# Performance work log

Hardware: AMD Instinct MI355X
Metric: run time of the kernel (lower is better)

## Reference

```python
import jax, jax.numpy as jnp
import numpy as np

NORM_EPS = 1e-6


def setup_inputs() -> dict:
    key = jax.random.key(0)
    k1, k2 = jax.random.split(key)
    in_features, out_features = 4096, 4096
    x = jax.random.normal(k1, (2, 2048, in_features), dtype=jnp.float32)
    scale = 1.0 / np.sqrt(in_features)
    weight = jax.random.normal(k2, (out_features, in_features), dtype=jnp.float32) * scale
    norm_weight = jnp.ones((in_features,), dtype=jnp.float32)
    return {"x": x, "weight": weight, "norm_weight": norm_weight}


def reference(x, weight, norm_weight):
    # RMSNorm over the last dim
    rms = jnp.sqrt(jnp.mean(x * x, axis=-1, keepdims=True) + NORM_EPS)
    x_n = x / rms * norm_weight
    # ternary weight quantization (absmean scale alpha)
    alpha = jnp.maximum(jnp.mean(jnp.abs(weight)), 1e-10)
    w_q = jnp.clip(jnp.round(weight / alpha), -1.0, 1.0)
    # per-token int8 activation quantization (absmax scale gamma)
    gamma = jnp.maximum(jnp.max(jnp.abs(x_n), axis=-1, keepdims=True), 1e-10)
    x_q = jnp.clip(jnp.round(x_n * 127.0 / gamma), -128.0, 127.0)
    # rescaled matmul: y = x_q @ w_q.T * (alpha * gamma / 127)
    y = jnp.einsum('bsk,nk->bsn', x_q, w_q) * (alpha * gamma / 127.0)
    return y
```

## Files before the change

kernel.cpp:

```cpp
#include <hip/hip_runtime.h>
#include <cstdint>
#include <cstddef>


#define KD 4096
#define MD 4096
#define ND 4096

#define WBLK 512

typedef int i32x4 __attribute__((ext_vector_type(4)));

__device__ __forceinline__ void gl2lds16(const signed char* g, signed char* l) {
  __builtin_amdgcn_global_load_lds(
      (const __attribute__((address_space(1))) void*)g,
      (__attribute__((address_space(3))) void*)l, 16, 0, 0);
}

__device__ __forceinline__ float wave_sum(float v) {
#pragma unroll
  for (int off = 32; off; off >>= 1) v += __shfl_down(v, off, 64);
  return v;
}
__device__ __forceinline__ float wave_max(float v) {
#pragma unroll
  for (int off = 32; off; off >>= 1) v = fmaxf(v, __shfl_down(v, off, 64));
  return v;
}


__global__ __launch_bounds__(256) void k_alpha_part(const float* __restrict__ w,
                                                    float* __restrict__ part) {
  __shared__ float red[4];
  const int tid = threadIdx.x;
  const float4* w4 = (const float4*)(w + (size_t)blockIdx.x * 4096);
  float s = 0.f;
#pragma unroll
  for (int i = 0; i < 4; ++i) {
    float4 v = w4[i * 256 + tid];
    s += fabsf(v.x) + fabsf(v.y) + fabsf(v.z) + fabsf(v.w);
  }
  s = wave_sum(s);
  if ((tid & 63) == 0) red[tid >> 6] = s;
  __syncthreads();
  if (tid == 0) part[blockIdx.x] = (red[0] + red[1]) + (red[2] + red[3]);
}


__device__ __forceinline__ uint32_t qw4(float4 v, float alpha) {
  int q0 = (int)fminf(fmaxf(rintf(v.x / alpha), -1.f), 1.f);
  int q1 = (int)fminf(fmaxf(rintf(v.y / alpha), -1.f), 1.f);
  int q2 = (int)fminf(fmaxf(rintf(v.z / alpha), -1.f), 1.f);
  int q3 = (int)fminf(fmaxf(rintf(v.w / alpha), -1.f), 1.f);
  return (uint32_t)(q0 & 255) | ((uint32_t)(q1 & 255) << 8) |
         ((uint32_t)(q2 & 255) << 16) | ((uint32_t)(q3 & 255) << 24);
}

__global__ __launch_bounds__(256) void k_quant_all(const float* __restrict__ w,
                                                   const float* __restrict__ x,
                                                   const float* __restrict__ nw,
                                                   const float* __restrict__ part,
                                                   signed char* __restrict__ wq,
                                                   signed char* __restrict__ xq,
                                                   float* __restrict__ gamma,
                                                   float* __restrict__ alpha_out) {
  const int tid = threadIdx.x;
  const int bid = blockIdx.x;
  __shared__ float red[4];
  __shared__ float red2[4];

  if (bid < 4096) {
    const int row = bid;
    const float4* x4 = (const float4*)(x + (size_t)row * 4096);
    const float4* n4 = (const float4*)nw;
    float4 xv[4], nv[4];
#pragma unroll
    for (int i = 0; i < 4; ++i) {
      xv[i] = x4[i * 256 + tid];
      nv[i] = n4[i * 256 + tid];
    }
    float ss = 0.f, mx = 0.f;
#pragma unroll
    for (int i = 0; i < 4; ++i) {
      ss += xv[i].x * xv[i].x + xv[i].y * xv[i].y + xv[i].z * xv[i].z +
            xv[i].w * xv[i].w;
      mx = fmaxf(mx,
                 fmaxf(fmaxf(fabsf(xv[i].x * nv[i].x), fabsf(xv[i].y * nv[i].y)),
                       fmaxf(fabsf(xv[i].z * nv[i].z), fabsf(xv[i].w * nv[i].w))));
    }
    ss = wave_sum(ss);
    mx = wave_max(mx);
    if ((tid & 63) == 0) {
      red[tid >> 6] = ss;
      red2[tid >> 6] = mx;
    }
    __syncthreads();
    const float tot = (red[0] + red[1]) + (red[2] + red[3]);
    const float rms = sqrtf(tot * (1.0f / 4096.0f) + 1e-6f);
    const float mxr = fmaxf(fmaxf(red2[0], red2[1]), fmaxf(red2[2], red2[3]));
    const float g = fmaxf(mxr / rms, 1e-10f);
    if (tid == 0) gamma[row] = g;
    const float inv = 127.0f / (rms * g);

    uint32_t* xqi = (uint32_t*)(xq + (size_t)row * 4096);
#pragma unroll
    for (int i = 0; i < 4; ++i) {
      const int f = i * 256 + tid;
      int q0 = (int)fminf(fmaxf(rintf(xv[i].x * nv[i].x * inv), -128.f), 127.f);
      int q1 = (int)fminf(fmaxf(rintf(xv[i].y * nv[i].y * inv), -128.f), 127.f);
      int q2 = (int)fminf(fmaxf(rintf(xv[i].z * nv[i].z * inv), -128.f), 127.f);
      int q3 = (int)fminf(fmaxf(rintf(xv[i].w * nv[i].w * inv), -128.f), 127.f);
      xqi[f] = (uint32_t)(q0 & 255) | ((uint32_t)(q1 & 255) << 8) |
               ((uint32_t)(q2 & 255) << 16) | ((uint32_t)(q3 & 255) << 24);
    }
  } else {
    const int wb = bid - 4096;
    float s = 0.f;
#pragma unroll
    for (int i = 0; i < 16; ++i) s += part[i * 256 + tid];
    s = wave_sum(s);
    if ((tid & 63) == 0) red[tid >> 6] = s;
    __syncthreads();
    const float alpha =
        fmaxf(((red[0] + red[1]) + (red[2] + red[3])) * (1.0f / 16777216.0f),
              1e-10f);
    if (wb == 0 && tid == 0) alpha_out[0] = alpha;

    const float4* w4 = (const float4*)w;
    uint32_t* wqi = (uint32_t*)wq;
#pragma unroll 1
    for (int k = 0; k < 32; k += 4) {
      const int f0 = (wb * 32 + k) * 256 + tid;
      float4 v0 = w4[f0];
      float4 v1 = w4[f0 + 256];
      float4 v2 = w4[f0 + 512];
      float4 v3 = w4[f0 + 768];
      wqi[f0] = qw4(v0, alpha);
      wqi[f0 + 256] = qw4(v1, alpha);
      wqi[f0 + 512] = qw4(v2, alpha);
      wqi[f0 + 768] = qw4(v3, alpha);
    }
  }
}


#define BM 256
#define BN 256
#define BK 64

__global__ __launch_bounds__(512, 2) void k_gemm(const signed char* __restrict__ xq,
                                                 const signed char* __restrict__ wq,
                                                 const float* __restrict__ gamma,
                                                 const float* __restrict__ alpha_p,
                                                 float* __restrict__ out) {
  __shared__ __align__(16) signed char LDS_[65536];
  const int tid = threadIdx.x;
  const int lane = tid & 63;
  const int wave = tid >> 6;
  const int wm = (wave >> 2) * 128;
  const int wn = (wave & 3) * 64;
  const int quad = lane >> 4;
  const int l16 = lane & 15;

  const int bid = (blockIdx.x & 7) * 32 + (blockIdx.x >> 3);
  const int bm = (bid >> 4) * BM;
  const int bn = (bid & 15) * BN;

  const int lr = lane >> 2;
  const int sc = (lane & 3) ^ ((lane >> 3) & 3);
  const int rb0 = wave * 16;
  const int rb1 = (8 + wave) * 16;
  const signed char* ag0 = xq + (size_t)(bm + rb0 + lr) * KD + sc * 16;
  const signed char* ag1 = xq + (size_t)(bm + rb1 + lr) * KD + sc * 16;
  const signed char* bg0 = wq + (size_t)(bn + rb0 + lr) * KD + sc * 16;
  const signed char* bg1 = wq + (size_t)(bn + rb1 + lr) * KD + sc * 16;
  const int lA0 = rb0 * BK;
  const int lA1 = rb1 * BK;

  const int pos = (quad ^ ((l16 >> 1) & 3)) * 16;

  i32x4 acc[8][4];
#pragma unroll
  for (int i = 0; i < 8; ++i)
#pragma unroll
    for (int j = 0; j < 4; ++j) acc[i][j] = (i32x4){0, 0, 0, 0};

  gl2lds16(ag0, LDS_ + lA0);
  gl2lds16(ag1, LDS_ + lA1);
  gl2lds16(bg0, LDS_ + 16384 + lA0);
  gl2lds16(bg1, LDS_ + 16384 + lA1);
  __syncthreads();

  for (int t = 0; t < 64; ++t) {
    const int c = t & 1;
    const signed char* Ab = LDS_ + c * 32768;
    const signed char* Bb = Ab + 16384;
    signed char* An = LDS_ + (c ^ 1) * 32768;
    signed char* Bn = An + 16384;
    const size_t kn = (size_t)(t + 1) * BK;
    const bool more = (t < 63);

    i32x4 bf[4], af[2];

#pragma unroll
    for (int p = 0; p < 4; ++p) {
      if (p == 0) {
#pragma unroll
        for (int ni = 0; ni < 4; ++ni)
          bf[ni] = *(const i32x4*)&Bb[(wn + ni * 16 + l16) * BK + pos];
      }
#pragma unroll
      for (int j = 0; j < 2; ++j)
        af[j] = *(const i32x4*)&Ab[(wm + (p * 2 + j) * 16 + l16) * BK + pos];

      if (more) {
        if (p == 0) {
          gl2lds16(ag0 + kn, An + lA0);
          gl2lds16(ag1 + kn, An + lA1);
        } else if (p == 1) {
          gl2lds16(bg0 + kn, Bn + lA0);
          gl2lds16(bg1 + kn, Bn + lA1);
        }
      }
      __builtin_amdgcn_s_barrier();
      __builtin_amdgcn_s_setprio(1);
#pragma unroll
      for (int j = 0; j < 2; ++j)
#pragma unroll
        for (int ni = 0; ni < 4; ++ni)
          acc[p * 2 + j][ni] = __builtin_amdgcn_mfma_i32_16x16x64_i8(
              af[j], bf[ni], acc[p * 2 + j][ni], 0, 0, 0);
      __builtin_amdgcn_s_setprio(0);
      if (p < 3) __builtin_amdgcn_s_barrier();
    }
    __syncthreads();
  }

  const float alpha = alpha_p[0];
#pragma unroll
  for (int mi = 0; mi < 8; ++mi) {
#pragma unroll
    for (int r = 0; r < 4; ++r) {
      const int m = bm + wm + mi * 16 + quad * 4 + r;
      const float s = (alpha * gamma[m]) / 127.0f;
#pragma unroll
      for (int ni = 0; ni < 4; ++ni) {
        const int n = bn + wn + ni * 16 + l16;
        out[(size_t)m * ND + n] = (float)acc[mi][ni][r] * s;
      }
    }
  }
}


extern "C" void kernel_launch(void* const* d_in, const int* in_sizes, int n_in,
                              void* d_out, int out_size, void* d_ws, size_t ws_size,
                              hipStream_t stream) {
  const float* x = (const float*)d_in[0];
  const float* w = (const float*)d_in[1];
  const float* nw = (const float*)d_in[2];
  float* out = (float*)d_out;

  char* ws = (char*)d_ws;
  signed char* xq = (signed char*)ws;
  signed char* wq = (signed char*)(ws + ((size_t)1 << 24));
  float* gamma = (float*)(ws + ((size_t)2 << 24));
  float* part = (float*)(ws + ((size_t)2 << 24) + 16384);
  float* alpha = (float*)(ws + ((size_t)2 << 24) + 32768);

  k_alpha_part<<<4096, 256, 0, stream>>>(w, part);
  k_quant_all<<<4096 + WBLK, 256, 0, stream>>>(w, x, nw, part, wq, xq, gamma, alpha);
  k_gemm<<<dim3(256), dim3(512), 0, stream>>>(xq, wq, gamma, alpha, out);
}
```

Measured before the change: 235.9 us.

## Software-pipeline LDS fragment loads and drop per-phase barriers in int8 GEMM loop

Register-prefetches the next A fragments one phase ahead and the next tile's B and A fragments at the last phase, so LDS reads overlap the MFMAs. The trailing barrier of each phase and the per-iteration __syncthreads are removed, and an explicit vmcnt(0) wait before the final barrier makes the next tile visible. This cuts synchronisation and LDS latency stalls in the main loop, at the cost of extra registers for the double-buffered fragments. It also risks write-after-read hazards on the LDS buffers now that fewer barriers separate reads from the next global-to-LDS writes.

```diff
diff --git a/kernel.cpp b/kernel.cpp
--- a/kernel.cpp
+++ b/kernel.cpp
@@ -185,34 +185,37 @@
 #pragma unroll
     for (int j = 0; j < 4; ++j) acc[i][j] = (i32x4){0, 0, 0, 0};
 
+  i32x4 bf[4], bfn[4], af[2][2];
+
   gl2lds16(ag0, LDS_ + lA0);
   gl2lds16(ag1, LDS_ + lA1);
   gl2lds16(bg0, LDS_ + 16384 + lA0);
   gl2lds16(bg1, LDS_ + 16384 + lA1);
   __syncthreads();
-
+#pragma unroll
+  for (int ni = 0; ni < 4; ++ni)
+    bf[ni] = *(const i32x4*)&LDS_[16384 + (wn + ni * 16 + l16) * BK + pos];
+#pragma unroll
+  for (int j = 0; j < 2; ++j)
+    af[0][j] = *(const i32x4*)&LDS_[(wm + j * 16 + l16) * BK + pos];
+
+#pragma unroll 2
   for (int t = 0; t < 64; ++t) {
     const int c = t & 1;
     const signed char* Ab = LDS_ + c * 32768;
-    const signed char* Bb = Ab + 16384;
     signed char* An = LDS_ + (c ^ 1) * 32768;
     signed char* Bn = An + 16384;
     const size_t kn = (size_t)(t + 1) * BK;
     const bool more = (t < 63);
 
-    i32x4 bf[4], af[2];
-
 #pragma unroll
     for (int p = 0; p < 4; ++p) {
-      if (p == 0) {
-#pragma unroll
-        for (int ni = 0; ni < 4; ++ni)
-          bf[ni] = *(const i32x4*)&Bb[(wn + ni * 16 + l16) * BK + pos];
-      }
-#pragma unroll
-      for (int j = 0; j < 2; ++j)
-        af[j] = *(const i32x4*)&Ab[(wm + (p * 2 + j) * 16 + l16) * BK + pos];
-
+      if (p < 3) {
+#pragma unroll
+        for (int j = 0; j < 2; ++j)
+          af[(p + 1) & 1][j] =
+              *(const i32x4*)&Ab[(wm + ((p + 1) * 2 + j) * 16 + l16) * BK + pos];
+      }
       if (more) {
         if (p == 0) {
           gl2lds16(ag0 + kn, An + lA0);
@@ -220,20 +223,32 @@
         } else if (p == 1) {
           gl2lds16(bg0 + kn, Bn + lA0);
           gl2lds16(bg1 + kn, Bn + lA1);
+        } else if (p == 3) {
+          asm volatile("s_waitcnt vmcnt(0)" ::: "memory");
         }
       }
       __builtin_amdgcn_s_barrier();
+      if (p == 3 && more) {
+#pragma unroll
+        for (int ni = 0; ni < 4; ++ni)
+          bfn[ni] = *(const i32x4*)&Bn[(wn + ni * 16 + l16) * BK + pos];
+#pragma unroll
+        for (int j = 0; j < 2; ++j)
+          af[0][j] = *(const i32x4*)&An[(wm + j * 16 + l16) * BK + pos];
+      }
       __builtin_amdgcn_s_setprio(1);
 #pragma unroll
       for (int j = 0; j < 2; ++j)
 #pragma unroll
         for (int ni = 0; ni < 4; ++ni)
           acc[p * 2 + j][ni] = __builtin_amdgcn_mfma_i32_16x16x64_i8(
-              af[j], bf[ni], acc[p * 2 + j][ni], 0, 0, 0);
+              af[p & 1][j], bf[ni], acc[p * 2 + j][ni], 0, 0, 0);
       __builtin_amdgcn_s_setprio(0);
-      if (p < 3) __builtin_amdgcn_s_barrier();
-    }
-    __syncthreads();
+      if (p == 3 && more) {
+#pragma unroll
+        for (int ni = 0; ni < 4; ++ni) bf[ni] = bfn[ni];
+      }
+    }
   }
 
   const float alpha = alpha_p[0];
```

Result: faster. 230.0 us (-2.5%).
